# Kernel tuning notes

Measured on AMD Instinct MI355X. Metric: run time of the kernel, lower is better.

## Reference

```python
import jax, jax.numpy as jnp
import numpy as np

N, IN_DIM, OUT_DIM, HEADS = 8192, 256, 128, 2


def setup_inputs() -> dict:
    key = jax.random.key(0)
    k1, k2, k3, k4, k5 = jax.random.split(key, 5)
    features = jax.random.normal(k1, (N, IN_DIM), dtype=jnp.float32)
    adjacency = jax.random.randint(k2, (N, N), 0, 2, dtype=jnp.int32)
    # nn.Linear(input_dim, output_dim*heads, bias=False): weight [out, in]
    W = jax.random.normal(k3, (OUT_DIM * HEADS, IN_DIM), dtype=jnp.float32) * 0.05
    attn_src = jax.random.normal(k4, (HEADS, OUT_DIM), dtype=jnp.float32) * 0.05
    attn_dst = jax.random.normal(k5, (HEADS, OUT_DIM), dtype=jnp.float32) * 0.05
    return {"features": features, "adjacency": adjacency, "W": W,
            "attn_src": attn_src, "attn_dst": attn_dst}


def reference(features, adjacency, W, attn_src, attn_dst):
    n = features.shape[0]
    # transformed: [N, H, F]
    transformed = (features @ W.T).reshape(n, HEADS, OUT_DIM)
    src_scores = jnp.einsum('nhf,hf->nh', transformed, attn_src)  # [N, H]
    dst_scores = jnp.einsum('nhf,hf->nh', transformed, attn_dst)  # [N, H]
    # logits: [N_src, N_dst, H]
    logits = jax.nn.leaky_relu(src_scores[:, None, :] + dst_scores[None, :, :],
                               negative_slope=0.2)
    mask = adjacency > 0  # [N, N]
    logits = jnp.where(mask[:, :, None], logits, -jnp.inf)
    attention = jax.nn.softmax(logits, axis=1)  # softmax over dst dim (dim=1)
    attention = jnp.nan_to_num(attention, nan=0.0, posinf=0.0, neginf=0.0)
    aggregated = jnp.einsum('ijh,jhf->ihf', attention, transformed)  # [N, H, F]
    return aggregated.mean(axis=1)  # [N, F]
```

## Files before the change

### kernel.cpp

```cpp
#include <hip/hip_runtime.h>
#include <stdint.h>
#include <stddef.h>

#define NN 8192
#define KD 256
#define CD 256
#define FD 128
#define BI 32
#define BJ 64

typedef __attribute__((ext_vector_type(4))) float f32x4;
typedef __attribute__((ext_vector_type(8))) short b16x8;

__device__ __forceinline__ unsigned short f2bf(float x) {
    unsigned int u = __float_as_uint(x);
    u += 0x7fffu + ((u >> 16) & 1u);
    return (unsigned short)(u >> 16);
}

__device__ __forceinline__ void async16(const void* g, void* l) {
    __builtin_amdgcn_global_load_lds(
        (const __attribute__((address_space(1))) unsigned int*)g,
        (__attribute__((address_space(3))) unsigned int*)l, 16, 0, 0);
}

__global__ __launch_bounds__(256) void k_transform(
    const float* __restrict__ feat, const float* __restrict__ W,
    const float* __restrict__ asrc, const float* __restrict__ adst,
    unsigned short* __restrict__ Tt, float* __restrict__ s, float* __restrict__ d)
{
    __shared__ unsigned short a_lds[64 * 32];
    __shared__ unsigned short b_lds[256 * 32];
    __shared__ unsigned short tr_lds[256 * 72];
    __shared__ float sc_lds[4][64];
    __shared__ float dc_lds[4][64];

    const int t = threadIdx.x;
    const int wave = t >> 6, lane = t & 63;
    const int l15 = lane & 15, quad = lane >> 4;
    const int n0 = blockIdx.x * 64;
    const int ai = t >> 2, ag = t & 3;

    f32x4 acc[4][4] = {};
    for (int kc = 0; kc < 8; ++kc) {
        const int k0 = kc * 32;
        __syncthreads();
        {
            const float* src = feat + (size_t)(n0 + ai) * KD + k0 + ag * 8;
            const float4 v0 = *(const float4*)src;
            const float4 v1 = *(const float4*)(src + 4);
            union { unsigned short us[8]; b16x8 v; } pk;
            pk.us[0] = f2bf(v0.x); pk.us[1] = f2bf(v0.y);
            pk.us[2] = f2bf(v0.z); pk.us[3] = f2bf(v0.w);
            pk.us[4] = f2bf(v1.x); pk.us[5] = f2bf(v1.y);
            pk.us[6] = f2bf(v1.z); pk.us[7] = f2bf(v1.w);
            const int slot = ag ^ ((ai >> 1) & 3);
            *(b16x8*)&a_lds[ai * 32 + slot * 8] = pk.v;
        }
        for (int p = 0; p < 4; ++p) {
            const int G = p * 256 + t;
            const int c = G >> 2, g = G & 3;
            const float* src = W + (size_t)c * KD + k0 + g * 8;
            const float4 v0 = *(const float4*)src;
            const float4 v1 = *(const float4*)(src + 4);
            union { unsigned short us[8]; b16x8 v; } pk;
            pk.us[0] = f2bf(v0.x); pk.us[1] = f2bf(v0.y);
            pk.us[2] = f2bf(v0.z); pk.us[3] = f2bf(v0.w);
            pk.us[4] = f2bf(v1.x); pk.us[5] = f2bf(v1.y);
            pk.us[6] = f2bf(v1.z); pk.us[7] = f2bf(v1.w);
            const int slot = g ^ ((c >> 1) & 3);
            *(b16x8*)&b_lds[c * 32 + slot * 8] = pk.v;
        }
        __syncthreads();
        b16x8 af[4], bfr[4];
        for (int mt = 0; mt < 4; ++mt) {
            const int m = mt * 16 + l15;
            af[mt] = *(const b16x8*)&a_lds[m * 32 + (quad ^ ((m >> 1) & 3)) * 8];
        }
        for (int nt = 0; nt < 4; ++nt) {
            const int c = wave * 64 + nt * 16 + l15;
            bfr[nt] = *(const b16x8*)&b_lds[c * 32 + (quad ^ ((c >> 1) & 3)) * 8];
        }
        for (int mt = 0; mt < 4; ++mt)
            for (int nt = 0; nt < 4; ++nt)
                acc[mt][nt] = __builtin_amdgcn_mfma_f32_16x16x32_bf16(
                    af[mt], bfr[nt], acc[mt][nt], 0, 0, 0);
    }

    float aS[4], aD[4];
    for (int nt = 0; nt < 4; ++nt) {
        const int c = wave * 64 + nt * 16 + l15;
        aS[nt] = asrc[c]; aD[nt] = adst[c];
    }
    for (int mt = 0; mt < 4; ++mt)
        for (int r = 0; r < 4; ++r) {
            float vs = 0.f, vd = 0.f;
            for (int nt = 0; nt < 4; ++nt) {
                const float x = acc[mt][nt][r];
                vs += x * aS[nt]; vd += x * aD[nt];
            }
            vs += __shfl_xor(vs, 1); vd += __shfl_xor(vd, 1);
            vs += __shfl_xor(vs, 2); vd += __shfl_xor(vd, 2);
            vs += __shfl_xor(vs, 4); vd += __shfl_xor(vd, 4);
            vs += __shfl_xor(vs, 8); vd += __shfl_xor(vd, 8);
            if (l15 == 0) {
                const int nl = mt * 16 + quad * 4 + r;
                sc_lds[wave][nl] = vs; dc_lds[wave][nl] = vd;
            }
        }
    for (int mt = 0; mt < 4; ++mt)
        for (int nt = 0; nt < 4; ++nt)
            for (int r = 0; r < 4; ++r) {
                const int c = wave * 64 + nt * 16 + l15;
                const int n = mt * 16 + quad * 4 + r;
                tr_lds[c * 72 + n] = f2bf(acc[mt][nt][r]);
            }
    __syncthreads();
    if (t < 128) {
        const int n = t >> 1, h = t & 1;
        s[(size_t)(n0 + n) * 2 + h] = sc_lds[h * 2][n] + sc_lds[h * 2 + 1][n];
        d[(size_t)(n0 + n) * 2 + h] = dc_lds[h * 2][n] + dc_lds[h * 2 + 1][n];
    }
    for (int p = 0; p < 8; ++p) {
        const int idx = p * 256 + t;
        const int c = idx >> 3, g = idx & 7;
        *(b16x8*)(Tt + (size_t)c * NN + n0 + g * 8) = *(const b16x8*)&tr_lds[c * 72 + g * 8];
    }
}

__global__ __launch_bounds__(256, 4) void k_gat(
    const int* __restrict__ adj, const unsigned short* __restrict__ Tt,
    const float* __restrict__ s, const float* __restrict__ d,
    float* __restrict__ num_part,
    float* __restrict__ den_part,
    int jchunk)
{
    __shared__ unsigned short tt_lds[CD * BJ];
    __shared__ unsigned short w_lds[2 * BI * BJ];

    const int t = threadIdx.x;
    const int wave = t >> 6, lane = t & 63;
    const int l15 = lane & 15, quad = lane >> 4;
    const int i0 = blockIdx.x * BI;
    const int chunk = blockIdx.y;
    const int jbase = chunk * jchunk;

    const int wi = t >> 3;
    const int j8 = t & 7;
    const int gi = i0 + wi;
    const float s0 = s[(size_t)gi * 2 + 0];
    const float s1 = s[(size_t)gi * 2 + 1];

    const int h = wave >> 1;
    const int fh = wave & 1;
    const int cbase = h * 128 + fh * 64;

    f32x4 acc[2][4] = {};
    float den0 = 0.f, den1 = 0.f;
    const int njt = jchunk / BJ;

    for (int jt = 0; jt < njt; ++jt) {
        const int j0 = jbase + jt * BJ;
        __syncthreads();
        const int* arow = adj + (size_t)gi * NN + j0 + j8 * 8;
        const int4 a0 = *(const int4*)arow;
        const int4 a1 = *(const int4*)(arow + 4);
        const float4* dvp = (const float4*)(d + (size_t)(j0 + j8 * 8) * 2);
        union { float4 v[4]; float f[16]; } dv;
        dv.v[0] = dvp[0]; dv.v[1] = dvp[1]; dv.v[2] = dvp[2]; dv.v[3] = dvp[3];
        for (int p = 0; p < 8; ++p) {
            const int G = (p * 4 + wave) * 64 + lane;
            const int c = G >> 3, gt = G & 7;
            const int g = gt ^ (c & 7);
            async16(Tt + (size_t)c * NN + j0 + g * 8,
                    (char*)tt_lds + (size_t)(p * 4 + wave) * 1024);
        }
        const int am[8] = {a0.x, a0.y, a0.z, a0.w, a1.x, a1.y, a1.z, a1.w};
        union { unsigned short us[8]; b16x8 v; } w0, w1;
        float dp0 = 0.f, dp1 = 0.f;
        for (int e = 0; e < 8; ++e) {
            float x0 = s0 + dv.f[e * 2 + 0];  x0 = x0 > 0.f ? x0 : 0.2f * x0;
            float x1 = s1 + dv.f[e * 2 + 1];  x1 = x1 > 0.f ? x1 : 0.2f * x1;
            const float e0 = am[e] != 0 ? __expf(x0) : 0.f;
            const float e1 = am[e] != 0 ? __expf(x1) : 0.f;
            dp0 += e0; dp1 += e1;
            w0.us[e] = f2bf(e0); w1.us[e] = f2bf(e1);
        }
        den0 += dp0; den1 += dp1;
        const int slot = (j8 ^ (wi & 7)) << 3;
        *(b16x8*)&w_lds[(0 * BI + wi) * BJ + slot] = w0.v;
        *(b16x8*)&w_lds[(1 * BI + wi) * BJ + slot] = w1.v;
        __syncthreads();
        for (int ks = 0; ks < 2; ++ks) {
            const int gidx = ks * 4 + quad;
            b16x8 af[2], bfr[4];
            for (int mt = 0; mt < 2; ++mt) {
                const int m = mt * 16 + l15;
                af[mt] = *(const b16x8*)&w_lds[(h * BI + m) * BJ + ((gidx ^ (m & 7)) << 3)];
            }
            for (int nt = 0; nt < 4; ++nt) {
                const int c = cbase + nt * 16 + l15;
                bfr[nt] = *(const b16x8*)&tt_lds[c * BJ + ((gidx ^ (c & 7)) << 3)];
            }
            for (int mt = 0; mt < 2; ++mt)
                for (int nt = 0; nt < 4; ++nt)
                    acc[mt][nt] = __builtin_amdgcn_mfma_f32_16x16x32_bf16(
                        af[mt], bfr[nt], acc[mt][nt], 0, 0, 0);
        }
    }
    den0 += __shfl_xor(den0, 1); den0 += __shfl_xor(den0, 2); den0 += __shfl_xor(den0, 4);
    den1 += __shfl_xor(den1, 1); den1 += __shfl_xor(den1, 2); den1 += __shfl_xor(den1, 4);
    if (j8 == 0) {
        den_part[((size_t)chunk * 2 + 0) * NN + gi] = den0;
        den_part[((size_t)chunk * 2 + 1) * NN + gi] = den1;
    }
    float* np_ = num_part + (size_t)chunk * NN * CD;
    for (int mt = 0; mt < 2; ++mt)
        for (int nt = 0; nt < 4; ++nt)
            for (int r = 0; r < 4; ++r) {
                const int n = i0 + mt * 16 + quad * 4 + r;
                const int c = cbase + nt * 16 + l15;
                np_[(size_t)n * CD + c] = acc[mt][nt][r];
            }
}

__global__ __launch_bounds__(256) void k_combine(
    const float* __restrict__ num_part, const float* __restrict__ den_part,
    float* __restrict__ out, int jsplit)
{
    const int idx = blockIdx.x * 256 + threadIdx.x;
    const int n = idx >> 7, f = idx & 127;
    const size_t row = (size_t)n * CD;
    float n0 = 0.f, n1 = 0.f, d0 = 0.f, d1 = 0.f;
    for (int c = 0; c < jsplit; ++c) {
        const size_t base = (size_t)c * NN * CD;
        n0 += num_part[base + row + f];
        n1 += num_part[base + row + 128 + f];
        d0 += den_part[((size_t)c * 2 + 0) * NN + n];
        d1 += den_part[((size_t)c * 2 + 1) * NN + n];
    }
    const float r0 = d0 != 0.f ? n0 / d0 : 0.f;
    const float r1 = d1 != 0.f ? n1 / d1 : 0.f;
    out[idx] = 0.5f * (r0 + r1);
}

extern "C" void kernel_launch(void* const* d_in, const int* in_sizes, int n_in,
                              void* d_out, int out_size, void* d_ws, size_t ws_size,
                              hipStream_t stream) {
    const float* feat = (const float*)d_in[0];
    const int*   adj  = (const int*)d_in[1];
    const float* W    = (const float*)d_in[2];
    const float* asrc = (const float*)d_in[3];
    const float* adst = (const float*)d_in[4];
    float* out = (float*)d_out;

    const int jsplit = (ws_size >= ((size_t)40 << 20)) ? 4 : 2;
    const int jchunk = NN / jsplit;

    char* ws = (char*)d_ws;
    unsigned short* Tt = (unsigned short*)ws;
    float* s    = (float*)(ws + ((size_t)4 << 20));
    float* dsc  = (float*)(ws + ((size_t)4 << 20) + (64 << 10));
    float* den  = (float*)(ws + ((size_t)4 << 20) + (128 << 10));
    float* nump = (float*)(ws + ((size_t)8 << 20));

    k_transform<<<128, 256, 0, stream>>>(feat, W, asrc, adst, Tt, s, dsc);
    k_gat<<<dim3(NN / BI, jsplit), 256, 0, stream>>>(adj, Tt, s, dsc, nump, den, jchunk);
    k_combine<<<NN * FD / 256, 256, 0, stream>>>(nump, den, out, jsplit);
}
```

Before: 462.6 us.

## Double-buffer GAT tiles and overlap exp/pack with MFMA via software pipeline

New measurement: 479.9 us. +3.7%, slower.

```diff
diff --git a/kernel.cpp b/kernel.cpp
--- a/kernel.cpp
+++ b/kernel.cpp
@@ -7,7 +7,7 @@
 #define CD 256
 #define FD 128
 #define BI 32
-#define BJ 64
+#define BJ 32
 
 typedef __attribute__((ext_vector_type(4))) float f32x4;
 typedef __attribute__((ext_vector_type(8))) short b16x8;
@@ -24,10 +24,41 @@
         (__attribute__((address_space(3))) unsigned int*)l, 16, 0, 0);
 }
 
+__device__ __forceinline__ float exp_pack_store(
+    const int4 a0, const int4 a1, const float4 d0, const float4 d1,
+    float sv, unsigned short* wdst)
+{
+    const int am[8] = {a0.x, a0.y, a0.z, a0.w, a1.x, a1.y, a1.z, a1.w};
+    const float dd[8] = {d0.x, d0.y, d0.z, d0.w, d1.x, d1.y, d1.z, d1.w};
+    const float ninf = __int_as_float(0xff800000);
+    float e[8]; float dp = 0.f;
+#pragma unroll
+    for (int k = 0; k < 8; ++k) {
+        float x = sv + dd[k];
+        x = fmaxf(x, 0.f) + 0.2f * fminf(x, 0.f);
+        x = am[k] != 0 ? x : ninf;
+        const float ev = __expf(x);
+        dp += ev; e[k] = ev;
+    }
+    union { unsigned short us[8]; b16x8 v; } pk;
+#if __has_builtin(__builtin_amdgcn_cvt_pk_bf16_f32)
+#pragma unroll
+    for (int k = 0; k < 4; ++k) {
+        auto p = __builtin_amdgcn_cvt_pk_bf16_f32(e[2 * k], e[2 * k + 1]);
+        __builtin_memcpy(&pk.us[2 * k], &p, 4);
+    }
+#else
+#pragma unroll
+    for (int k = 0; k < 8; ++k) pk.us[k] = f2bf(e[k]);
+#endif
+    *(b16x8*)wdst = pk.v;
+    return dp;
+}
+
 __global__ __launch_bounds__(256) void k_transform(
     const float* __restrict__ feat, const float* __restrict__ W,
     const float* __restrict__ asrc, const float* __restrict__ adst,
-    unsigned short* __restrict__ Tt, float* __restrict__ s, float* __restrict__ d)
+    unsigned short* __restrict__ Tt, float* __restrict__ s_t, float* __restrict__ d_t)
 {
     __shared__ unsigned short a_lds[64 * 32];
     __shared__ unsigned short b_lds[256 * 32];
@@ -118,8 +149,8 @@
     __syncthreads();
     if (t < 128) {
         const int n = t >> 1, h = t & 1;
-        s[(size_t)(n0 + n) * 2 + h] = sc_lds[h * 2][n] + sc_lds[h * 2 + 1][n];
-        d[(size_t)(n0 + n) * 2 + h] = dc_lds[h * 2][n] + dc_lds[h * 2 + 1][n];
+        s_t[(size_t)h * NN + n0 + n] = sc_lds[h * 2][n] + sc_lds[h * 2 + 1][n];
+        d_t[(size_t)h * NN + n0 + n] = dc_lds[h * 2][n] + dc_lds[h * 2 + 1][n];
     }
     for (int p = 0; p < 8; ++p) {
         const int idx = p * 256 + t;
@@ -130,90 +161,99 @@
 
 __global__ __launch_bounds__(256, 4) void k_gat(
     const int* __restrict__ adj, const unsigned short* __restrict__ Tt,
-    const float* __restrict__ s, const float* __restrict__ d,
+    const float* __restrict__ s_t, const float* __restrict__ d_t,
     float* __restrict__ num_part,
     float* __restrict__ den_part,
-    int jchunk)
+    int njt)
 {
-    __shared__ unsigned short tt_lds[CD * BJ];
-    __shared__ unsigned short w_lds[2 * BI * BJ];
+    __shared__ unsigned short tt_lds[2][256 * 32];
+    __shared__ unsigned short w_lds[2][2][32][32];
 
     const int t = threadIdx.x;
     const int wave = t >> 6, lane = t & 63;
     const int l15 = lane & 15, quad = lane >> 4;
     const int i0 = blockIdx.x * BI;
     const int chunk = blockIdx.y;
-    const int jbase = chunk * jchunk;
-
-    const int wi = t >> 3;
-    const int j8 = t & 7;
+    const size_t jbase = (size_t)chunk * njt * BJ;
+
+    const int eh = t >> 7;
+    const int wi = (t & 127) >> 2;
+    const int g4 = t & 3;
     const int gi = i0 + wi;
-    const float s0 = s[(size_t)gi * 2 + 0];
-    const float s1 = s[(size_t)gi * 2 + 1];
-
-    const int h = wave >> 1;
-    const int fh = wave & 1;
-    const int cbase = h * 128 + fh * 64;
+    const float sv = s_t[(size_t)eh * NN + gi];
+    const int wslot = (g4 ^ ((wi >> 1) & 3)) * 8;
+
+    const int mh = wave >> 1, fh = wave & 1;
+    const int cbase = mh * 128 + fh * 64;
 
     f32x4 acc[2][4] = {};
-    float den0 = 0.f, den1 = 0.f;
-    const int njt = jchunk / BJ;
+    float den = 0.f;
+
+    const int* ap = adj + (size_t)gi * NN + jbase + g4 * 8;
+    const float* dp_ = d_t + (size_t)eh * NN + jbase + g4 * 8;
+
+    for (int p = 0; p < 4; ++p) {
+        const int G = (p * 4 + wave) * 64 + lane;
+        const int c = G >> 2;
+        const int g = (G & 3) ^ ((c >> 1) & 3);
+        async16(Tt + (size_t)c * NN + jbase + g * 8,
+                (char*)&tt_lds[0][0] + (size_t)(p * 4 + wave) * 1024);
+    }
+    __builtin_amdgcn_sched_barrier(0);
+    int4 cA0 = ((const int4*)ap)[0], cA1 = ((const int4*)ap)[1];
+    float4 cD0 = ((const float4*)dp_)[0], cD1 = ((const float4*)dp_)[1];
+    {
+        const int j1 = (njt > 1) ? BJ : 0;
+        int4 nA0 = *(const int4*)(ap + j1);
+        int4 nA1 = *(const int4*)(ap + j1 + 4);
+        float4 nD0 = *(const float4*)(dp_ + j1);
+        float4 nD1 = *(const float4*)(dp_ + j1 + 4);
+        den += exp_pack_store(cA0, cA1, cD0, cD1, sv, &w_lds[0][eh][wi][wslot]);
+        cA0 = nA0; cA1 = nA1; cD0 = nD0; cD1 = nD1;
+    }
+    asm volatile("s_waitcnt vmcnt(4) lgkmcnt(0)\n\ts_barrier" ::: "memory");
 
     for (int jt = 0; jt < njt; ++jt) {
-        const int j0 = jbase + jt * BJ;
-        __syncthreads();
-        const int* arow = adj + (size_t)gi * NN + j0 + j8 * 8;
-        const int4 a0 = *(const int4*)arow;
-        const int4 a1 = *(const int4*)(arow + 4);
-        const float4* dvp = (const float4*)(d + (size_t)(j0 + j8 * 8) * 2);
-        union { float4 v[4]; float f[16]; } dv;
-        dv.v[0] = dvp[0]; dv.v[1] = dvp[1]; dv.v[2] = dvp[2]; dv.v[3] = dvp[3];
-        for (int p = 0; p < 8; ++p) {
+        const int cur = jt & 1, nxt = cur ^ 1;
+        b16x8 af[2], bfr[4];
+        for (int mt = 0; mt < 2; ++mt) {
+            const int m = mt * 16 + l15;
+            af[mt] = *(const b16x8*)&w_lds[cur][mh][m][(quad ^ ((m >> 1) & 3)) * 8];
+        }
+        for (int nt = 0; nt < 4; ++nt) {
+            const int c = cbase + nt * 16 + l15;
+            bfr[nt] = *(const b16x8*)&tt_lds[cur][c * 32 + (quad ^ ((c >> 1) & 3)) * 8];
+        }
+        const size_t jnext = jbase + (size_t)((jt + 1 < njt) ? jt + 1 : jt) * BJ;
+        for (int p = 0; p < 4; ++p) {
             const int G = (p * 4 + wave) * 64 + lane;
-            const int c = G >> 3, gt = G & 7;
-            const int g = gt ^ (c & 7);
-            async16(Tt + (size_t)c * NN + j0 + g * 8,
-                    (char*)tt_lds + (size_t)(p * 4 + wave) * 1024);
-        }
-        const int am[8] = {a0.x, a0.y, a0.z, a0.w, a1.x, a1.y, a1.z, a1.w};
-        union { unsigned short us[8]; b16x8 v; } w0, w1;
-        float dp0 = 0.f, dp1 = 0.f;
-        for (int e = 0; e < 8; ++e) {
-            float x0 = s0 + dv.f[e * 2 + 0];  x0 = x0 > 0.f ? x0 : 0.2f * x0;
-            float x1 = s1 + dv.f[e * 2 + 1];  x1 = x1 > 0.f ? x1 : 0.2f * x1;
-            const float e0 = am[e] != 0 ? __expf(x0) : 0.f;
-            const float e1 = am[e] != 0 ? __expf(x1) : 0.f;
-            dp0 += e0; dp1 += e1;
-            w0.us[e] = f2bf(e0); w1.us[e] = f2bf(e1);
-        }
-        den0 += dp0; den1 += dp1;
-        const int slot = (j8 ^ (wi & 7)) << 3;
-        *(b16x8*)&w_lds[(0 * BI + wi) * BJ + slot] = w0.v;
-        *(b16x8*)&w_lds[(1 * BI + wi) * BJ + slot] = w1.v;
-        __syncthreads();
-        for (int ks = 0; ks < 2; ++ks) {
-            const int gidx = ks * 4 + quad;
-            b16x8 af[2], bfr[4];
-            for (int mt = 0; mt < 2; ++mt) {
-                const int m = mt * 16 + l15;
-                af[mt] = *(const b16x8*)&w_lds[(h * BI + m) * BJ + ((gidx ^ (m & 7)) << 3)];
-            }
-            for (int nt = 0; nt < 4; ++nt) {
-                const int c = cbase + nt * 16 + l15;
-                bfr[nt] = *(const b16x8*)&tt_lds[c * BJ + ((gidx ^ (c & 7)) << 3)];
-            }
-            for (int mt = 0; mt < 2; ++mt)
-                for (int nt = 0; nt < 4; ++nt)
-                    acc[mt][nt] = __builtin_amdgcn_mfma_f32_16x16x32_bf16(
-                        af[mt], bfr[nt], acc[mt][nt], 0, 0, 0);
-        }
-    }
-    den0 += __shfl_xor(den0, 1); den0 += __shfl_xor(den0, 2); den0 += __shfl_xor(den0, 4);
-    den1 += __shfl_xor(den1, 1); den1 += __shfl_xor(den1, 2); den1 += __shfl_xor(den1, 4);
-    if (j8 == 0) {
-        den_part[((size_t)chunk * 2 + 0) * NN + gi] = den0;
-        den_part[((size_t)chunk * 2 + 1) * NN + gi] = den1;
-    }
+            const int c = G >> 2;
+            const int g = (G & 3) ^ ((c >> 1) & 3);
+            async16(Tt + (size_t)c * NN + jnext + g * 8,
+                    (char*)&tt_lds[nxt][0] + (size_t)(p * 4 + wave) * 1024);
+        }
+        __builtin_amdgcn_sched_barrier(0);
+        const int j2 = (((jt + 2 < njt) ? jt + 2 : njt - 1)) * BJ;
+        int4 nA0 = *(const int4*)(ap + j2);
+        int4 nA1 = *(const int4*)(ap + j2 + 4);
+        float4 nD0 = *(const float4*)(dp_ + j2);
+        float4 nD1 = *(const float4*)(dp_ + j2 + 4);
+        const float dpv = exp_pack_store(cA0, cA1, cD0, cD1, sv,
+                                         &w_lds[nxt][eh][wi][wslot]);
+        if (jt + 1 < njt) den += dpv;
+        for (int mt = 0; mt < 2; ++mt)
+            for (int nt = 0; nt < 4; ++nt)
+                acc[mt][nt] = __builtin_amdgcn_mfma_f32_16x16x32_bf16(
+                    af[mt], bfr[nt], acc[mt][nt], 0, 0, 0);
+        cA0 = nA0; cA1 = nA1; cD0 = nD0; cD1 = nD1;
+        asm volatile("s_waitcnt vmcnt(4) lgkmcnt(0)\n\ts_barrier" ::: "memory");
+    }
+
+    float dv = den;
+    dv += __shfl_xor(dv, 1); dv += __shfl_xor(dv, 2);
+    if (g4 == 0)
+        den_part[((size_t)chunk * 2 + eh) * NN + gi] = dv;
+
     float* np_ = num_part + (size_t)chunk * NN * CD;
     for (int mt = 0; mt < 2; ++mt)
         for (int nt = 0; nt < 4; ++nt)
@@ -255,16 +295,16 @@
     float* out = (float*)d_out;
 
     const int jsplit = (ws_size >= ((size_t)40 << 20)) ? 4 : 2;
-    const int jchunk = NN / jsplit;
+    const int njt = (NN / jsplit) / BJ;
 
     char* ws = (char*)d_ws;
     unsigned short* Tt = (unsigned short*)ws;
-    float* s    = (float*)(ws + ((size_t)4 << 20));
-    float* dsc  = (float*)(ws + ((size_t)4 << 20) + (64 << 10));
+    float* s_t  = (float*)(ws + ((size_t)4 << 20));
+    float* d_t  = (float*)(ws + ((size_t)4 << 20) + (64 << 10));
     float* den  = (float*)(ws + ((size_t)4 << 20) + (128 << 10));
     float* nump = (float*)(ws + ((size_t)8 << 20));
 
-    k_transform<<<128, 256, 0, stream>>>(feat, W, asrc, adst, Tt, s, dsc);
-    k_gat<<<dim3(NN / BI, jsplit), 256, 0, stream>>>(adj, Tt, s, dsc, nump, den, jchunk);
+    k_transform<<<128, 256, 0, stream>>>(feat, W, asrc, adst, Tt, s_t, d_t);
+    k_gat<<<dim3(NN / BI, jsplit), 256, 0, stream>>>(adj, Tt, s_t, d_t, nump, den, njt);
     k_combine<<<NN * FD / 256, 256, 0, stream>>>(nump, den, out, jsplit);
 }
```
